# Performance work log

Measured on AMD Instinct MI355X. Metric: run time of the kernel, lower is better.

## Reference

```python
import jax, jax.numpy as jnp
import numpy as np

B, T, D = 64, 64, 64
E, HA, HB, OUT = 128, 128, 128, 1
SHORT = 2


def _rn(k, shape, scale=0.05):
    return jax.random.normal(k, shape, dtype=jnp.float32) * scale


def setup_inputs() -> dict:
    key = jax.random.key(0)
    ks = jax.random.split(key, 18)
    return {
        "x": jax.random.normal(ks[0], (B, T, D), dtype=jnp.float32),
        "W_emb": _rn(ks[1], (E, D)), "b_emb": _rn(ks[2], (E,)),
        "Wi_a": _rn(ks[3], (3 * HA, E)), "Wh_a": _rn(ks[4], (3 * HA, HA)),
        "bi_a": _rn(ks[5], (3 * HA,)), "bh_a": _rn(ks[6], (3 * HA,)),
        "Wi_b": _rn(ks[7], (3 * HB, E)), "Wh_b": _rn(ks[8], (3 * HB, HB)),
        "bi_b": _rn(ks[9], (3 * HB,)), "bh_b": _rn(ks[10], (3 * HB,)),
        "Wa": _rn(ks[11], (1, HA)), "ba": _rn(ks[12], (1,)),
        "Wb": _rn(ks[13], (E, HB)), "bb": _rn(ks[14], (E,)),
        "Wo": _rn(ks[15], (OUT, E)), "bo": _rn(ks[16], (OUT,)),
        "short": SHORT,
    }


def _gru_cell(x, h, Wi, Wh, bi, bh):
    # PyTorch GRU cell: gates ordered (r, z, n)
    gi = x @ Wi.T + bi
    gh = h @ Wh.T + bh
    ir, iz, in_ = jnp.split(gi, 3, axis=-1)
    hr, hz, hn = jnp.split(gh, 3, axis=-1)
    r = jax.nn.sigmoid(ir + hr)
    z = jax.nn.sigmoid(iz + hz)
    n = jnp.tanh(in_ + r * hn)
    return (1.0 - z) * n + z * h


def _forward(x, W_emb, b_emb, Wi_a, Wh_a, bi_a, bh_a, Wi_b, Wh_b, bi_b, bh_b,
             Wa, ba, Wb, bb, Wo, bo, short):
    Bn, Tn = x.shape[0], x.shape[1]
    temp = jnp.transpose(x, (1, 0, 2))            # [T, B, D]
    emb = temp @ W_emb.T + b_emb                  # [T, B, E]
    P = Tn - 1                                    # prefix p handles att_timesteps t = p+1
    S = Tn - 1                                    # max reversed-prefix length
    p_idx = jnp.arange(P)
    h0a = jnp.zeros((P, Bn, Wh_a.shape[1]), x.dtype)
    h0b = jnp.zeros((P, Bn, Wh_b.shape[1]), x.dtype)

    # All prefixes at once: for prefix p, reversed input at step s is emb[p - s].
    def step(carry, s):
        ha, hb = carry
        j = jnp.clip(p_idx - s, 0, Tn - 1)        # [P]
        e_in = emb[j]                             # [P, B, E]
        x_in = temp[j]                            # [P, B, D]
        na = _gru_cell(e_in, ha, Wi_a, Wh_a, bi_a, bh_a)
        nb = _gru_cell(e_in, hb, Wi_b, Wh_b, bi_b, bh_b)
        valid = (p_idx >= s)[:, None, None]
        ha = jnp.where(valid, na, ha)
        hb = jnp.where(valid, nb, hb)
        return (ha, hb), (ha, hb, e_in, x_in)

    _, (Ha, Hb, Eg, Xg) = jax.lax.scan(step, (h0a, h0b), jnp.arange(S))
    Ha = 0.5 * Ha                                 # reverse_h_a * 0.5, [S, P, B, HA]
    Hb = 0.5 * Hb                                 # reverse_h_b * 0.5, [S, P, B, HB]

    mask = p_idx[None, :] >= jnp.arange(S)[:, None]   # [S, P] valid scan steps
    preA = jnp.einsum('spbh,h->spb', Ha, Wa[0]) + ba[0]
    preA = jnp.where(mask[:, :, None], preA, -jnp.inf)
    alpha = jax.nn.softmax(preA, axis=0)              # softmax over prefix positions
    beta = jnp.tanh(jnp.einsum('spbh,eh->spbe', Hb, Wb) + bb)  # [S, P, B, E]

    # context: c[p] = sum_s alpha * beta * emb[p-s]  (softmax is order-invariant)
    c = jnp.einsum('spb,spbe->pbe', alpha, beta * Eg)          # [P, B, E]
    pred = c @ Wo.T + bo                                        # [P, B, 1]

    # interpretability weights: e = (beta * w_out) @ W_emb, f = alpha*e*x, g = mean over prefix
    e_chain = jnp.einsum('spbe,ed->spbd', beta * Wo[0], W_emb)  # [S, P, B, D]
    f = alpha[..., None] * e_chain * Xg
    g = jnp.sum(f, axis=0) / (p_idx[:, None, None] + 1.0)       # mean over t = p+1 steps

    pred = jnp.transpose(pred[short + 1:], (1, 0, 2))           # [B, T-2-short, 1]
    weight = jnp.transpose(g[short + 1:], (1, 0, 2))            # [B, T-2-short, D]
    return pred, weight


def reference(x, W_emb, b_emb, Wi_a, Wh_a, bi_a, bh_a, Wi_b, Wh_b, bi_b, bh_b,
              Wa, ba, Wb, bb, Wo, bo, short):
    return _forward(x, W_emb, b_emb, Wi_a, Wh_a, bi_a, bh_a, Wi_b, Wh_b, bi_b,
                    bh_b, Wa, ba, Wb, bb, Wo, bo, short)
```

## Files before the change

kernel.cpp:

```cpp
#include <hip/hip_runtime.h>
#include <hip/hip_bf16.h>
#include <math.h>

#define B_ 64
#define T_ 64
#define D_ 64
#define PMIN 3
#define NPOUT 60
#define NCHUNK 8

#define LOG2E     1.4426950408889634f
#define TWOLOG2E  2.8853900817779268f

typedef __hip_bfloat16 bf16;
typedef __attribute__((ext_vector_type(4))) short s16x4;
typedef __attribute__((ext_vector_type(8))) short s16x8;
typedef __attribute__((ext_vector_type(4))) float f32x4;

#define OFF_EMB   0
#define OFF_WIC2  524288
#define OFF_XT    622592
#define OFF_GIPK  884736
#define OFF_WPK   2457600
#define OFF_BPPK  2506752
#define OFF_WMPK  2514944
#define OFF_WALPK 2519040
#define OFF_FLAG  2520064

__device__ __forceinline__ float bf2f(unsigned short u) {
    union { float f; unsigned u32; } x; x.u32 = ((unsigned)u) << 16; return x.f;
}
__device__ __forceinline__ unsigned short f2bf(float f) {
    union { float f; unsigned u; } x; x.f = f;
    unsigned r = x.u + 0x7FFFu + ((x.u >> 16) & 1u);
    return (unsigned short)(r >> 16);
}
__device__ __forceinline__ float LDF(const void* p, int i, int flag) {
    return flag ? ((const float*)p)[i] : bf2f(((const unsigned short*)p)[i]);
}
__device__ __forceinline__ float sig2(float xneg) {
    return __builtin_amdgcn_rcpf(1.f + __builtin_exp2f(xneg));
}
__device__ __forceinline__ float tanh2(float x2) {
    return 1.f - 2.f * __builtin_amdgcn_rcpf(1.f + __builtin_exp2f(x2));
}
__device__ __forceinline__ int kpi(int s) {
    return (s & ~31) | ((s & 1) << 4) | ((s & 31) >> 1);
}

__global__ void detect_dtype(const unsigned short* xr, int* flag)
{
    int tid = threadIdx.x;
    int bad = 0;
    for (int i = tid; i < 4096; i += 256) {
        int ex = (xr[i] >> 7) & 0xFF;
        if (ex >= 140) bad++;
    }
    __shared__ int s[256];
    s[tid] = bad;
    __syncthreads();
    for (int st = 128; st > 0; st >>= 1) {
        if (tid < st) s[tid] += s[tid + st];
        __syncthreads();
    }
    if (tid == 0) *flag = (s[0] > 4) ? 1 : 0;
}

__global__ void prep_all(const void* p_x, const void* p_wemb,
                         const void* p_wia, const void* p_wib,
                         const void* p_wha, const void* p_whb,
                         const void* p_wa, const void* p_wb, const void* p_wo,
                         float* ws, const int* flagp)
{
    const int flag = *flagp;
    int id = blockIdx.x * 256 + threadIdx.x;
    if (id < 98304) {
        float v = (id < 49152) ? LDF(p_wia, id, flag)
                               : LDF(p_wib, id - 49152, flag);
        ws[OFF_WIC2 + id] = v;
    } else if (id < 360448) {
        int id5 = id - 98304;
        int b = id5 & 63, d = (id5 >> 6) & 63, t = id5 >> 12;
        ws[OFF_XT + id5] = LDF(p_x, (b * 64 + t) * 64 + d, flag);
    } else if (id < 458752) {
        unsigned short* wpk = (unsigned short*)(ws + OFF_WPK);
        int id3 = id - 360448;
        int w = id3 / 12288, r1 = id3 % 12288;
        int nt = r1 / 2048, r2 = r1 % 2048;
        int kt = r2 / 512, r3 = r2 % 512;
        int lane = r3 >> 3, j = r3 & 7;
        int cell = w >> 2, wv = w & 3;
        int gate = nt >> 1, tt = nt & 1;
        int g = gate * 128 + wv * 32 + tt * 16 + (lane & 15);
        int k = kpi(kt * 32 + (lane >> 4) * 8 + j);
        float sc = (gate < 2) ? -LOG2E : TWOLOG2E;
        wpk[id3] = f2bf(sc * LDF(cell ? p_whb : p_wha, g * 128 + k, flag));
    } else if (id < 475136) {
        unsigned short* bpk = (unsigned short*)(ws + OFF_BPPK);
        int id4 = id - 458752;
        int w = id4 / 2048, r = id4 % 2048;
        int kt = r / 512, lane = (r % 512) >> 3, j = r & 7;
        int e = w * 16 + (lane & 15);
        int k = kpi(kt * 32 + (lane >> 4) * 8 + j);
        bpk[id4] = f2bf(LOG2E * LDF(p_wb, e * 128 + k, flag));
    } else if (id < 483328) {
        unsigned short* wmk = (unsigned short*)(ws + OFF_WMPK);
        int id6 = id - 475136;
        int nt = id6 / 2048, r = id6 % 2048;
        int kt = r / 512, lane = (r % 512) >> 3, j = r & 7;
        int d = nt * 16 + (lane & 15);
        int e = kt * 32 + (lane >> 4) * 8 + j;
        wmk[id6] = f2bf(LDF(p_wo, e, flag) * LDF(p_wemb, e * 64 + d, flag));
    } else {
        unsigned short* alk = (unsigned short*)(ws + OFF_WALPK);
        int id7 = id - 483328;
        int kt = id7 / 512, lane = (id7 % 512) >> 3, j = id7 & 7;
        int k = kpi(kt * 32 + (lane >> 4) * 8 + j);
        alk[id7] = ((lane & 15) == 0) ? f2bf(0.5f * LOG2E * LDF(p_wa, k, flag))
                                      : (unsigned short)0;
    }
}

__global__ void prep_gi(float* ws, const void* p_x, const void* p_wemb,
                        const void* p_bemb, const void* p_bia, const void* p_bha,
                        const void* p_bib, const void* p_bhb, const int* flagp)
{
    const int flag = *flagp;
    unsigned short* gipk = (unsigned short*)(ws + OFF_GIPK);
    int t = blockIdx.x >> 3;
    int chunk = blockIdx.x & 7;
    int b0 = chunk * 8;
    int tid = threadIdx.x;
    __shared__ __align__(16) float sX[8][64];
    __shared__ __align__(16) float sWe[128][64];
    __shared__ __align__(16) float semT2[8][132];
    __shared__ __align__(16) unsigned short stg[6144];

    for (int i = tid; i < 512; i += 256) {
        int r = i >> 6, d = i & 63;
        sX[r][d] = LDF(p_x, ((b0 + r) * 64 + t) * 64 + d, flag);
    }
    for (int i = tid; i < 8192; i += 256)
        sWe[i >> 6][i & 63] = LDF(p_wemb, i, flag);
    __syncthreads();

    #pragma unroll
    for (int q = 0; q < 4; q++) {
        int o = tid + q * 256;
        int e = o & 127, r = o >> 7;
        float acc = LDF(p_bemb, e, flag);
        #pragma unroll
        for (int d = 0; d < 64; d += 4) {
            f32x4 xv = *(const f32x4*)&sX[r][d];
            f32x4 wv = *(const f32x4*)&sWe[e][d];
            acc += xv[0]*wv[0] + xv[1]*wv[1] + xv[2]*wv[2] + xv[3]*wv[3];
        }
        semT2[r][e] = acc;
        ws[OFF_EMB + (size_t)((t * 64 + b0 + r) * 128) + e] = acc;
    }
    __syncthreads();

    float acc3[3][8];
    #pragma unroll
    for (int g3 = 0; g3 < 3; g3++)
        #pragma unroll
        for (int r = 0; r < 8; r++) acc3[g3][r] = 0.f;
    const float* w2 = ws + OFF_WIC2;
    #pragma unroll 2
    for (int e0 = 0; e0 < 128; e0 += 4) {
        f32x4 wv0 = *(const f32x4*)(w2 + (size_t)(tid      ) * 128 + e0);
        f32x4 wv1 = *(const f32x4*)(w2 + (size_t)(tid + 256) * 128 + e0);
        f32x4 wv2 = *(const f32x4*)(w2 + (size_t)(tid + 512) * 128 + e0);
        f32x4 h[8];
        #pragma unroll
        for (int r = 0; r < 8; r++) h[r] = *(const f32x4*)&semT2[r][e0];
        #pragma unroll
        for (int r = 0; r < 8; r++)
            #pragma unroll
            for (int c = 0; c < 4; c++) {
                acc3[0][r] += wv0[c] * h[r][c];
                acc3[1][r] += wv1[c] * h[r][c];
                acc3[2][r] += wv2[c] * h[r][c];
            }
    }
    #pragma unroll
    for (int g3 = 0; g3 < 3; g3++) {
        int g = tid + g3 * 256;
        int cellg = g / 384, gr = g % 384;
        int gate = gr / 128, kh = gr % 128;
        int wvp = kh / 32, tt2 = (kh % 32) / 16, l15p = kh % 16;
        int wq = cellg * 4 + wvp;
        float bias = LDF(cellg ? p_bib : p_bia, gr, flag);
        if (gate < 2) bias += LDF(cellg ? p_bhb : p_bha, gr, flag);
        float sc = (gate < 2) ? -LOG2E : TWOLOG2E;
        #pragma unroll
        for (int r = 0; r < 8; r++) {
            float v = sc * (acc3[g3][r] + bias);
            int lane2 = (r >> 2) * 16 + l15p;
            int slot = gate * 8 + tt2 * 4 + (r & 3);
            stg[(wq * 32 + lane2) * 24 + slot] = f2bf(v);
        }
    }
    __syncthreads();
    const uint4* s4 = (const uint4*)stg;
    uint4* d4 = (uint4*)(gipk + (size_t)(t * 8 + chunk) * 6144);
    for (int i = tid; i < 768; i += 256) d4[i] = s4[i];
}


__launch_bounds__(512, 2)
__global__ void chain_kernel(const float* ws, void* outv, const int* flagp,
                             const void* p_bha, const void* p_bhb,
                             const void* p_bb, const void* p_ba,
                             const void* p_bo, const void* p_wo)
{
    const int p = PMIN + (NPOUT - 1) - (int)blockIdx.x / NCHUNK;
    const int chunk = (int)blockIdx.x % NCHUNK;
    const int tid = threadIdx.x;
    const int lane = tid & 63;
    const int w = tid >> 6;
    const int cell = w >> 2;
    const int wv = w & 3;
    const int l15 = lane & 15;
    const int quad = lane >> 4;
    const int tt = quad >> 1;
    const int rquad = quad & 1;

    __shared__ __align__(16) short hbf[2][2][16][136];
    __shared__ __align__(16) short betbf[2][16][136];
    __shared__ __align__(16) short sWm[4][4][64][8];
    __shared__ float spaLds[2][8];

    const unsigned short* gipk = (const unsigned short*)(ws + OFF_GIPK);
    const unsigned short* wpk  = (const unsigned short*)(ws + OFF_WPK);
    const unsigned short* bpk  = (const unsigned short*)(ws + OFF_BPPK);
    const unsigned short* alk  = (const unsigned short*)(ws + OFF_WALPK);
    const int flag = *flagp;

    {
        const int* s2 = (const int*)(ws + OFF_WMPK);
        int* d2 = (int*)&sWm[0][0][0][0];
        for (int i = tid; i < 4096; i += 512) d2[i] = s2[i];
        int* hz = (int*)&hbf[0][0][0][0];
        for (int i = tid; i < 4352; i += 512) hz[i] = 0;
        int* bz = (int*)&betbf[0][0][0];
        for (int i = tid; i < 2176; i += 512) bz[i] = 0;
    }

    s16x8 wB[6][4];
    #pragma unroll
    for (int nt = 0; nt < 6; nt++)
        #pragma unroll
        for (int kt = 0; kt < 4; kt++)
            wB[nt][kt] = *(const s16x8*)(wpk + (((w * 6 + nt) * 4 + kt) * 64 + lane) * 8);
    s16x8 bBp[4], wAl[4];
    #pragma unroll
    for (int kt = 0; kt < 4; kt++) {
        bBp[kt] = *(const s16x8*)(bpk + ((w * 4 + kt) * 64 + lane) * 8);
        wAl[kt] = *(const s16x8*)(alk + (kt * 64 + lane) * 8);
    }

    const float bhnS = TWOLOG2E *
        LDF(cell ? p_bhb : p_bha, 256 + wv * 32 + tt * 16 + l15, flag);
    const float bbE2 = TWOLOG2E * LDF(p_bb, w * 16 + l15, flag);
    const float bafS = LOG2E * LDF(p_ba, 0, flag);
    const float bof  = LDF(p_bo, 0, flag);

    float h_old[4];
    #pragma unroll
    for (int i = 0; i < 4; i++) h_old[i] = 0.f;
    float accR[9];
    #pragma unroll
    for (int i = 0; i < 9; i++) accR[i] = 0.f;

    __syncthreads();

    for (int it = 0; it <= p + 1; it++) {
        const int j = p - it;
        const int jp = j + 1;
        const bool doGru = (j >= 0);
        const bool doAcc = (it > 0);
        const int cur = it & 1;
        const int nxt = cur ^ 1;
        const int dbuf = it & 1;

        s16x4 giv[3];
        if (doGru) {
            const unsigned short* gp0 =
                gipk + ((((size_t)j * 8 + chunk) * 8 + w) * 32 + (lane & 31)) * 24;
            giv[0] = *(const s16x4*)(gp0 + tt * 4);
            giv[1] = *(const s16x4*)(gp0 + 8 + tt * 4);
            giv[2] = *(const s16x4*)(gp0 + 16 + tt * 4);
        }
        f32x4 xv, em0, em1;
        if (doAcc) {
            if (w < 4) {
                xv = *(const f32x4*)(ws + OFF_XT + ((size_t)jp * 64 + w * 16 + l15) * 64
                                     + chunk * 8 + rquad * 4);
            } else {
                const int row8 = (quad * 4 + (w - 4)) & 7;
                const float* ep = ws + OFF_EMB
                                  + ((size_t)jp * 64 + chunk * 8 + row8) * 128 + l15 * 8;
                em0 = *(const f32x4*)ep;
                em1 = *(const f32x4*)(ep + 4);
            }
        }

        f32x4 Cg[6], Cbp, Cal;
        #pragma unroll
        for (int nt = 0; nt < 6; nt++) Cg[nt] = (f32x4){0.f,0.f,0.f,0.f};
        Cbp = (f32x4){0.f,0.f,0.f,0.f};
        Cal = (f32x4){0.f,0.f,0.f,0.f};

        #pragma unroll
        for (int kt = 0; kt < 4; kt++) {
            s16x8 aB = *(const s16x8*)&hbf[cur][1][l15][kt * 32 + quad * 8];
            s16x8 aA;
            if (cell == 0 || w == 7) aA = *(const s16x8*)&hbf[cur][0][l15][kt * 32 + quad * 8];
            else aA = aB;
            s16x8 aOwn = cell ? aB : aA;
            #pragma unroll
            for (int nt = 0; nt < 6; nt++)
                Cg[nt] = __builtin_amdgcn_mfma_f32_16x16x32_bf16(aOwn, wB[nt][kt], Cg[nt], 0, 0, 0);
            Cbp = __builtin_amdgcn_mfma_f32_16x16x32_bf16(aB, bBp[kt], Cbp, 0, 0, 0);
            if (w == 7)
                Cal = __builtin_amdgcn_mfma_f32_16x16x32_bf16(aA, wAl[kt], Cal, 0, 0, 0);
        }

        if (w == 7 && l15 == 0 && quad < 2) {
            #pragma unroll
            for (int reg = 0; reg < 4; reg++)
                spaLds[dbuf][quad * 4 + reg] = fminf(Cal[reg] + bafS, 86.f);
        }
        if (doGru) {
            #pragma unroll
            for (int reg = 0; reg < 4; reg++) {
                float s1 = __shfl_xor(Cg[1][reg], 32);
                float s3 = __shfl_xor(Cg[3][reg], 32);
                float s5 = __shfl_xor(Cg[5][reg], 32);
                float ghr = tt ? s1 : Cg[0][reg];
                float ghz = tt ? s3 : Cg[2][reg];
                float ghn = (tt ? s5 : Cg[4][reg]) + bhnS;
                float gir = bf2f((unsigned short)giv[0][reg]);
                float giz = bf2f((unsigned short)giv[1][reg]);
                float gin = bf2f((unsigned short)giv[2][reg]);
                float rr = sig2(gir + ghr);
                float zz = sig2(giz + ghz);
                float nn = tanh2(gin + rr * ghn);
                float hv2 = (1.f - zz) * nn + zz * h_old[reg];
                h_old[reg] = hv2;
                hbf[nxt][cell][rquad * 4 + reg][wv * 32 + l15 * 2 + tt] = (short)f2bf(hv2);
            }
        }
        if (quad < 2) {
            #pragma unroll
            for (int reg = 0; reg < 4; reg++) {
                float bv = tanh2(Cbp[reg] + bbE2);
                betbf[dbuf][quad * 4 + reg][w * 16 + l15] = (short)f2bf(bv);
            }
        }

        __syncthreads();

        if (doAcc) {
            if (w < 4) {
                f32x4 ec = (f32x4){0.f,0.f,0.f,0.f};
                #pragma unroll
                for (int kt = 0; kt < 4; kt++) {
                    s16x8 a = *(const s16x8*)&betbf[dbuf][l15][kt * 32 + quad * 8];
                    s16x8 bw = *(const s16x8*)&sWm[w][kt][lane][0];
                    ec = __builtin_amdgcn_mfma_f32_16x16x32_bf16(a, bw, ec, 0, 0, 0);
                }
                #pragma unroll
                for (int reg = 0; reg < 4; reg++) {
                    float we = __builtin_exp2f(spaLds[dbuf][(quad * 4 + reg) & 7]);
                    accR[4 + reg] += we;
                    accR[reg] += we * ec[reg] * xv[reg];
                }
            } else {
                const int row8 = (quad * 4 + (w - 4)) & 7;
                float we = __builtin_exp2f(spaLds[dbuf][row8]);
                accR[8] += we;
                const short* bp2 = &betbf[dbuf][row8][l15 * 8];
                s16x4 blo = *(const s16x4*)bp2;
                s16x4 bhi = *(const s16x4*)(bp2 + 4);
                #pragma unroll
                for (int v = 0; v < 4; v++)
                    accR[v] += we * bf2f((unsigned short)blo[v]) * em0[v];
                #pragma unroll
                for (int v = 0; v < 4; v++)
                    accR[4 + v] += we * bf2f((unsigned short)bhi[v]) * em1[v];
            }
        }
    }

    if (w >= 4) {
        const int row = quad * 4 + (w - 4);
        float wo8[8];
        if (flag) {
            const float* wp = (const float*)p_wo + l15 * 8;
            #pragma unroll
            for (int v = 0; v < 8; v++) wo8[v] = wp[v];
        } else {
            const unsigned short* wp = (const unsigned short*)p_wo + l15 * 8;
            #pragma unroll
            for (int v = 0; v < 8; v++) wo8[v] = bf2f(wp[v]);
        }
        float part = 0.f;
        #pragma unroll
        for (int v = 0; v < 8; v++) part += accR[v] * wo8[v];
        part += __shfl_xor(part, 1);
        part += __shfl_xor(part, 2);
        part += __shfl_xor(part, 4);
        part += __shfl_xor(part, 8);
        if (l15 == 0 && row < 8) {
            int bglob = chunk * 8 + row;
            float pr = part / accR[8] + bof;
            size_t oi = (size_t)bglob * NPOUT + (p - PMIN);
            if (flag) ((float*)outv)[oi] = pr;
            else      ((bf16*)outv)[oi] = __float2bfloat16(pr);
        }
    } else if (quad < 2) {
        const float invt = 1.f / (float)(p + 1);
        #pragma unroll
        for (int reg = 0; reg < 4; reg++) {
            int row = quad * 4 + reg;
            int bglob = chunk * 8 + row;
            float gv = accR[reg] / accR[4 + reg] * invt;
            size_t oi = (size_t)B_ * NPOUT
                      + ((size_t)bglob * NPOUT + (p - PMIN)) * 64 + w * 16 + l15;
            if (flag) ((float*)outv)[oi] = gv;
            else      ((bf16*)outv)[oi] = __float2bfloat16(gv);
        }
    }
}

extern "C" void kernel_launch(void* const* d_in, const int* in_sizes, int n_in,
                              void* d_out, int out_size, void* d_ws, size_t ws_size,
                              hipStream_t stream)
{
    float* ws = (float*)d_ws;
    int* flagp = (int*)(ws + OFF_FLAG);

    hipLaunchKernelGGL(detect_dtype, dim3(1), dim3(256), 0, stream,
                       (const unsigned short*)d_in[0], flagp);
    hipLaunchKernelGGL(prep_all, dim3(1896), dim3(256), 0, stream,
                       d_in[0], d_in[1], d_in[3], d_in[7], d_in[4], d_in[8],
                       d_in[11], d_in[13], d_in[15], ws, flagp);
    hipLaunchKernelGGL(prep_gi, dim3(512), dim3(256), 0, stream,
                       ws, d_in[0], d_in[1], d_in[2], d_in[5], d_in[6],
                       d_in[9], d_in[10], flagp);
    hipLaunchKernelGGL(chain_kernel, dim3(NPOUT * NCHUNK), dim3(512), 0, stream,
                       ws, d_out, flagp,
                       d_in[6], d_in[10], d_in[14], d_in[12], d_in[16], d_in[15]);
}
```

Measured before the change: 304.8 us.

## Process 16 batch rows per chain block instead of 8, halving block count

The chain kernel now handles 16 batch rows per block (NCHUNK 4), so all 16 rows of each 16x16 MFMA tile are used instead of only 8. The GRU epilogue no longer needs cross-lane shuffles: each lane computes both hidden halves and packs them with a single bf16 pack instruction into LDS. The gate-input precompute kernel writes a new interleaved layout so each lane loads 8-wide vectors. This halves the number of blocks and the redundant MFMA work, at the cost of more per-thread register state and fewer blocks to spread across CUs.

```diff
diff --git a/kernel.cpp b/kernel.cpp
--- a/kernel.cpp
+++ b/kernel.cpp
@@ -7,7 +7,7 @@
 #define D_ 64
 #define PMIN 3
 #define NPOUT 60
-#define NCHUNK 8
+#define NCHUNK 4
 
 #define LOG2E     1.4426950408889634f
 #define TWOLOG2E  2.8853900817779268f
@@ -203,8 +203,12 @@
     }
     __syncthreads();
     const uint4* s4 = (const uint4*)stg;
-    uint4* d4 = (uint4*)(gipk + (size_t)(t * 8 + chunk) * 6144);
-    for (int i = tid; i < 768; i += 256) d4[i] = s4[i];
+    const int c16 = chunk >> 1, rhalf = chunk & 1;
+    uint4* d4 = (uint4*)(gipk + (size_t)(t * 4 + c16) * 12288);
+    for (int i = tid; i < 768; i += 256) {
+        int wq = i / 96, rem = i % 96;
+        d4[wq * 192 + rhalf * 96 + rem] = s4[i];
+    }
 }
 
 
@@ -223,13 +227,11 @@
     const int wv = w & 3;
     const int l15 = lane & 15;
     const int quad = lane >> 4;
-    const int tt = quad >> 1;
-    const int rquad = quad & 1;
 
     __shared__ __align__(16) short hbf[2][2][16][136];
     __shared__ __align__(16) short betbf[2][16][136];
     __shared__ __align__(16) short sWm[4][4][64][8];
-    __shared__ float spaLds[2][8];
+    __shared__ float spaLds[2][16];
 
     const unsigned short* gipk = (const unsigned short*)(ws + OFF_GIPK);
     const unsigned short* wpk  = (const unsigned short*)(ws + OFF_WPK);
@@ -260,15 +262,17 @@
         wAl[kt] = *(const s16x8*)(alk + (kt * 64 + lane) * 8);
     }
 
-    const float bhnS = TWOLOG2E *
-        LDF(cell ? p_bhb : p_bha, 256 + wv * 32 + tt * 16 + l15, flag);
+    const float bhnS0 = TWOLOG2E *
+        LDF(cell ? p_bhb : p_bha, 256 + wv * 32 + l15, flag);
+    const float bhnS1 = TWOLOG2E *
+        LDF(cell ? p_bhb : p_bha, 256 + wv * 32 + 16 + l15, flag);
     const float bbE2 = TWOLOG2E * LDF(p_bb, w * 16 + l15, flag);
     const float bafS = LOG2E * LDF(p_ba, 0, flag);
     const float bof  = LDF(p_bo, 0, flag);
 
-    float h_old[4];
-    #pragma unroll
-    for (int i = 0; i < 4; i++) h_old[i] = 0.f;
+    float h_old[8];
+    #pragma unroll
+    for (int i = 0; i < 8; i++) h_old[i] = 0.f;
     float accR[9];
     #pragma unroll
     for (int i = 0; i < 9; i++) accR[i] = 0.f;
@@ -284,23 +288,23 @@
         const int nxt = cur ^ 1;
         const int dbuf = it & 1;
 
-        s16x4 giv[3];
+        s16x8 giv[3];
         if (doGru) {
             const unsigned short* gp0 =
-                gipk + ((((size_t)j * 8 + chunk) * 8 + w) * 32 + (lane & 31)) * 24;
-            giv[0] = *(const s16x4*)(gp0 + tt * 4);
-            giv[1] = *(const s16x4*)(gp0 + 8 + tt * 4);
-            giv[2] = *(const s16x4*)(gp0 + 16 + tt * 4);
+                gipk + ((((size_t)j * 4 + chunk) * 8 + w) * 64 + lane) * 24;
+            giv[0] = *(const s16x8*)(gp0);
+            giv[1] = *(const s16x8*)(gp0 + 8);
+            giv[2] = *(const s16x8*)(gp0 + 16);
         }
         f32x4 xv, em0, em1;
         if (doAcc) {
             if (w < 4) {
                 xv = *(const f32x4*)(ws + OFF_XT + ((size_t)jp * 64 + w * 16 + l15) * 64
-                                     + chunk * 8 + rquad * 4);
+                                     + chunk * 16 + quad * 4);
             } else {
-                const int row8 = (quad * 4 + (w - 4)) & 7;
+                const int row = quad * 4 + (w - 4);
                 const float* ep = ws + OFF_EMB
-                                  + ((size_t)jp * 64 + chunk * 8 + row8) * 128 + l15 * 8;
+                                  + ((size_t)jp * 64 + chunk * 16 + row) * 128 + l15 * 8;
                 em0 = *(const f32x4*)ep;
                 em1 = *(const f32x4*)(ep + 4);
             }
@@ -327,7 +331,7 @@
                 Cal = __builtin_amdgcn_mfma_f32_16x16x32_bf16(aA, wAl[kt], Cal, 0, 0, 0);
         }
 
-        if (w == 7 && l15 == 0 && quad < 2) {
+        if (w == 7 && l15 == 0) {
             #pragma unroll
             for (int reg = 0; reg < 4; reg++)
                 spaLds[dbuf][quad * 4 + reg] = fminf(Cal[reg] + bafS, 86.f);
@@ -335,24 +339,24 @@
         if (doGru) {
             #pragma unroll
             for (int reg = 0; reg < 4; reg++) {
-                float s1 = __shfl_xor(Cg[1][reg], 32);
-                float s3 = __shfl_xor(Cg[3][reg], 32);
-                float s5 = __shfl_xor(Cg[5][reg], 32);
-                float ghr = tt ? s1 : Cg[0][reg];
-                float ghz = tt ? s3 : Cg[2][reg];
-                float ghn = (tt ? s5 : Cg[4][reg]) + bhnS;
-                float gir = bf2f((unsigned short)giv[0][reg]);
-                float giz = bf2f((unsigned short)giv[1][reg]);
-                float gin = bf2f((unsigned short)giv[2][reg]);
-                float rr = sig2(gir + ghr);
-                float zz = sig2(giz + ghz);
-                float nn = tanh2(gin + rr * ghn);
-                float hv2 = (1.f - zz) * nn + zz * h_old[reg];
-                h_old[reg] = hv2;
-                hbf[nxt][cell][rquad * 4 + reg][wv * 32 + l15 * 2 + tt] = (short)f2bf(hv2);
+                float rr0 = sig2(bf2f((unsigned short)giv[0][reg]) + Cg[0][reg]);
+                float zz0 = sig2(bf2f((unsigned short)giv[1][reg]) + Cg[2][reg]);
+                float nn0 = tanh2(bf2f((unsigned short)giv[2][reg])
+                                  + rr0 * (Cg[4][reg] + bhnS0));
+                float h0 = (1.f - zz0) * nn0 + zz0 * h_old[reg];
+                h_old[reg] = h0;
+                float rr1 = sig2(bf2f((unsigned short)giv[0][4 + reg]) + Cg[1][reg]);
+                float zz1 = sig2(bf2f((unsigned short)giv[1][4 + reg]) + Cg[3][reg]);
+                float nn1 = tanh2(bf2f((unsigned short)giv[2][4 + reg])
+                                  + rr1 * (Cg[5][reg] + bhnS1));
+                float h1 = (1.f - zz1) * nn1 + zz1 * h_old[4 + reg];
+                h_old[4 + reg] = h1;
+                unsigned pk;
+                asm("v_cvt_pk_bf16_f32 %0, %1, %2" : "=v"(pk) : "v"(h0), "v"(h1));
+                *(unsigned*)&hbf[nxt][cell][quad * 4 + reg][wv * 32 + l15 * 2] = pk;
             }
         }
-        if (quad < 2) {
+        {
             #pragma unroll
             for (int reg = 0; reg < 4; reg++) {
                 float bv = tanh2(Cbp[reg] + bbE2);
@@ -373,15 +377,15 @@
                 }
                 #pragma unroll
                 for (int reg = 0; reg < 4; reg++) {
-                    float we = __builtin_exp2f(spaLds[dbuf][(quad * 4 + reg) & 7]);
+                    float we = __builtin_exp2f(spaLds[dbuf][quad * 4 + reg]);
                     accR[4 + reg] += we;
                     accR[reg] += we * ec[reg] * xv[reg];
                 }
             } else {
-                const int row8 = (quad * 4 + (w - 4)) & 7;
-                float we = __builtin_exp2f(spaLds[dbuf][row8]);
+                const int row = quad * 4 + (w - 4);
+                float we = __builtin_exp2f(spaLds[dbuf][row]);
                 accR[8] += we;
-                const short* bp2 = &betbf[dbuf][row8][l15 * 8];
+                const short* bp2 = &betbf[dbuf][row][l15 * 8];
                 s16x4 blo = *(const s16x4*)bp2;
                 s16x4 bhi = *(const s16x4*)(bp2 + 4);
                 #pragma unroll
@@ -413,19 +417,19 @@
         part += __shfl_xor(part, 2);
         part += __shfl_xor(part, 4);
         part += __shfl_xor(part, 8);
-        if (l15 == 0 && row < 8) {
-            int bglob = chunk * 8 + row;
+        if (l15 == 0) {
+            int bglob = chunk * 16 + row;
             float pr = part / accR[8] + bof;
             size_t oi = (size_t)bglob * NPOUT + (p - PMIN);
             if (flag) ((float*)outv)[oi] = pr;
             else      ((bf16*)outv)[oi] = __float2bfloat16(pr);
         }
-    } else if (quad < 2) {
+    } else {
         const float invt = 1.f / (float)(p + 1);
         #pragma unroll
         for (int reg = 0; reg < 4; reg++) {
             int row = quad * 4 + reg;
-            int bglob = chunk * 8 + row;
+            int bglob = chunk * 16 + row;
             float gv = accR[reg] / accR[4 + reg] * invt;
             size_t oi = (size_t)B_ * NPOUT
                       + ((size_t)bglob * NPOUT + (p - PMIN)) * 64 + w * 16 + l15;
```

Result: slower. 318.9 us (+4.6%).
